# Kernel optimization log

Measured on AMD Instinct MI355X. Metric: run time of the kernel, lower is better.

## Reference

```python
import jax, jax.numpy as jnp
import numpy as np
from math import log

T, B, IN, H1, H2, OUT = 128, 256, 1024, 2048, 2048, 512
DT, INIT_TAU, MIN_TAU, THRESH, VREST = 0.01, 0.5, 0.1, 1.0, 0.0
SLOPE = 25.0  # snntorch surrogate.fast_sigmoid default slope

@jax.custom_vjp
def spike_fn(x):
    # Heaviside forward; fast-sigmoid surrogate backward
    return (x > 0).astype(x.dtype)

def _spike_fwd(x):
    return spike_fn(x), x

def _spike_bwd(x, g):
    return (g / (SLOPE * jnp.abs(x) + 1.0) ** 2,)

spike_fn.defvjp(_spike_fwd, _spike_bwd)

def setup_inputs() -> dict:
    key = jax.random.key(0)
    ks = jax.random.split(key, 7)
    init_w = -log(1.0 / (INIT_TAU - MIN_TAU) - 1.0)
    def lin(k, fan_in, fan_out):
        bound = 1.0 / np.sqrt(fan_in)
        kw, kb = jax.random.split(k)
        W = jax.random.uniform(kw, (fan_out, fan_in), jnp.float32, -bound, bound)
        b = jax.random.uniform(kb, (fan_out,), jnp.float32, -bound, bound)
        return W, b
    W1, b1 = lin(ks[0], IN, H1)
    W2, b2 = lin(ks[1], H1, H2)
    W3, b3 = lin(ks[2], H2, OUT)
    s = (jax.random.uniform(ks[3], (T, B, IN), jnp.float32) < 0.2).astype(jnp.float32)
    return {
        "s": s,
        "W1": W1, "b1": b1, "wt1": jnp.full((H1,), init_w, jnp.float32),
        "W2": W2, "b2": b2, "wt2": jnp.full((H2,), init_w, jnp.float32),
        "W3": W3, "b3": b3, "wt3": jnp.full((OUT,), init_w, jnp.float32),
    }

def _lif(v, cur, w_tau):
    tau = MIN_TAU + jax.nn.sigmoid(w_tau)
    v = v + (DT / tau) * (-(v - VREST) + cur)  # r = 1.0
    spike = spike_fn(v - THRESH)
    v_post = v * (1.0 - spike)  # zero reset
    return v_post, spike, v  # v is pre-reset membrane (v_tmp)

def reference(s, W1, b1, wt1, W2, b2, wt2, W3, b3, wt3):
    v0 = (jnp.zeros((B, H1), s.dtype), jnp.zeros((B, H2), s.dtype), jnp.zeros((B, OUT), s.dtype))
    def step(carry, st):
        v1, v2, v3 = carry
        v1, s1, _ = _lif(v1, st @ W1.T + b1, wt1)
        v2, s2, _ = _lif(v2, s1 @ W2.T + b2, wt2)
        v3, s3, vtmp = _lif(v3, s2 @ W3.T + b3, wt3)
        return (v1, v2, v3), (s3, vtmp)
    _, (out_s, out_v) = jax.lax.scan(step, v0, s)
    return out_s, out_v
```

## Files before the change

kernel.cpp:

```cpp
#include <hip/hip_runtime.h>
#include <hip/hip_bf16.h>
#include <cstdint>
#include <cstddef>

#define T_STEPS 128
#define BATCH   256
#define IN_F    1024
#define H1_F    2048
#define H2_F    2048
#define OUT_F   512
#define M_TOT   (T_STEPS * BATCH)

#define W1_SCALE 4064.0f
#define W1_INV   (1.0f / 4064.0f)

typedef __attribute__((ext_vector_type(4))) int   int4v;
typedef __attribute__((ext_vector_type(8))) unsigned short ushort8;
typedef unsigned long long ull;

__device__ __forceinline__ void load16_to_lds(const void* g, void* l) {
  __builtin_amdgcn_global_load_lds(
      (const __attribute__((address_space(1))) void*)g,
      (__attribute__((address_space(3))) void*)l, 16, 0, 0);
}

__device__ __forceinline__ unsigned short f2bf(float x) {
  __hip_bfloat16 h = __float2bfloat16(x);
  return *reinterpret_cast<unsigned short*>(&h);
}

__device__ __forceinline__ float bf2f(unsigned short u) {
  unsigned int w = ((unsigned int)u) << 16;
  return *reinterpret_cast<float*>(&w);
}

__device__ __forceinline__ float lif_k(float w) {
  float tau = 0.1f + 1.0f / (1.0f + expf(-w));
  return 0.01f / tau;
}

__global__ __launch_bounds__(256) void cvt_both(
    const float4* __restrict__ s_in, int4* __restrict__ s_out, int s16,
    const float4* __restrict__ w_in, int4* __restrict__ w_out, int w16) {
  int i = threadIdx.x + blockIdx.x * 256;
  bool is_s = (i < s16);
  const float4* in;
  int4* out;
  if (is_s) { in = s_in + (size_t)i * 4; out = s_out + i; }
  else {
    int j = i - s16;
    if (j >= w16) return;
    in = w_in + (size_t)j * 4; out = w_out + j;
  }
  int4 o;
  int* op = (int*)&o;
#pragma unroll
  for (int q = 0; q < 4; ++q) {
    float4 v = in[q];
    int c0, c1, c2, c3;
    if (is_s) {
      c0 = v.x > 0.5f; c1 = v.y > 0.5f; c2 = v.z > 0.5f; c3 = v.w > 0.5f;
    } else {
      c0 = __float2int_rn(v.x * W1_SCALE); c1 = __float2int_rn(v.y * W1_SCALE);
      c2 = __float2int_rn(v.z * W1_SCALE); c3 = __float2int_rn(v.w * W1_SCALE);
    }
    op[q] = (c0 & 0xff) | ((c1 & 0xff) << 8) | ((c2 & 0xff) << 16) | ((c3 & 0xff) << 24);
  }
  *out = o;
}

union SMem {
  struct { uint4 lA[1024]; uint4 lB[1024]; } st;
  unsigned short tile[128 * 136];
};

__global__ __launch_bounds__(256) void gemm_scan(
    const int8_t* __restrict__ A, const int8_t* __restrict__ B,
    const float* __restrict__ b1, const float* __restrict__ wt1,
    ull* __restrict__ mask1) {
  __shared__ SMem sm;
  const int K = IN_F;
  const int tid = threadIdx.x, lane = tid & 63, wv = tid >> 6;
  const int wm = (wv & 1) * 64, wn = (wv >> 1) * 64;

  const int id = blockIdx.x;
  const int xcd = id & 7, j = id >> 3;
  const int bblk = xcd * 32 + (j >> 4);
  const int n0   = (j & 15) * 128;

  const int mk = lane & 15, grp = lane >> 4;

  int4v acc[4][4] = {};

  for (int kt = 0; kt < K; kt += 128) {
#pragma unroll
    for (int i = 0; i < 4; ++i) {
      int cellbase = (wv * 4 + i) * 64;
      int cell = cellbase + lane;
      int r  = cell >> 3;
      int kb = (cell & 7) ^ (r & 7);
      load16_to_lds(A + (size_t)(r * BATCH + bblk) * K + kt + kb * 16, &sm.st.lA[cellbase]);
      load16_to_lds(B + (size_t)(n0 + r) * K + kt + kb * 16, &sm.st.lB[cellbase]);
    }
    __syncthreads();
#pragma unroll
    for (int ks = 0; ks < 2; ++ks) {
      int4v af[4], bfr[4];
      const int kb = ks * 4 + grp;
#pragma unroll
      for (int f = 0; f < 4; ++f) {
        int m = wm + f * 16 + mk;
        af[f]  = *(const int4v*)&sm.st.lA[m * 8 + (kb ^ (m & 7))];
        int n = wn + f * 16 + mk;
        bfr[f] = *(const int4v*)&sm.st.lB[n * 8 + (kb ^ (n & 7))];
      }
#pragma unroll
      for (int i = 0; i < 4; ++i)
#pragma unroll
        for (int jj = 0; jj < 4; ++jj)
          acc[i][jj] = __builtin_amdgcn_mfma_i32_16x16x64_i8(af[i], bfr[jj], acc[i][jj], 0, 0, 0);
    }
    __syncthreads();
  }

#pragma unroll
  for (int jj = 0; jj < 4; ++jj) {
    const int h = wn + jj * 16 + mk;
#pragma unroll
    for (int i = 0; i < 4; ++i) {
      const int t0 = wm + i * 16 + grp * 4;
      uint2 pk;
      pk.x = ((unsigned int)f2bf((float)acc[i][jj][1] * W1_INV) << 16)
           | f2bf((float)acc[i][jj][0] * W1_INV);
      pk.y = ((unsigned int)f2bf((float)acc[i][jj][3] * W1_INV) << 16)
           | f2bf((float)acc[i][jj][2] * W1_INV);
      *(uint2*)&sm.tile[h * 136 + t0] = pk;
    }
  }
  __syncthreads();

  if (tid < 128) {
    const int h  = tid;
    const int hg = n0 + h;
    const int wv2 = tid >> 6;
    const int ln  = tid & 63;
    const float bias = b1[hg];
    const float k    = lif_k(wt1[hg]);
    const size_t wbase = (size_t)(n0 >> 6) + wv2;
    float v = 0.0f;
    for (int t8 = 0; t8 < T_STEPS; t8 += 8) {
      ushort8 pk = *(const ushort8*)&sm.tile[h * 136 + t8];
#pragma unroll
      for (int u = 0; u < 8; ++u) {
        v = fmaf(k, (bf2f(pk[u]) + bias) - v, v);
        bool sp = v > 1.0f;
        ull bm = __ballot(sp);
        if (ln == 0)
          mask1[((size_t)(t8 + u) * BATCH + bblk) * (H1_F / 64) + wbase] = bm;
        if (sp) v = 0.0f;
      }
    }
  }
}

__global__ __launch_bounds__(1024) void layer23_kernel(
    const ull* __restrict__ mask1,
    const float* __restrict__ W2, const float* __restrict__ b2, const float* __restrict__ wt2,
    const float* __restrict__ W3, const float* __restrict__ b3, const float* __restrict__ wt3,
    float* __restrict__ out_s, float* __restrict__ out_v) {
  __shared__ ull m1all[T_STEPS * 32];
  __shared__ ull m2sh[2][32];
  const int tid = threadIdx.x, b = blockIdx.x;
  const int lane = tid & 63, wv = tid >> 6;

  const float bias2a = b2[tid], bias2b = b2[tid + 1024];
  const float k2a = lif_k(wt2[tid]), k2b = lif_k(wt2[tid + 1024]);
  const float* W2a = W2 + (size_t)tid * H1_F;
  const float* W2b = W2 + (size_t)(tid + 1024) * H1_F;
  float v2a = 0.0f, v2b = 0.0f;

  float bias3 = 0.0f, k3 = 0.0f, v3 = 0.0f;
  const float* W3r = W3;
  if (wv < 8) {
    bias3 = b3[tid];
    k3 = lif_k(wt3[tid]);
    W3r = W3 + (size_t)tid * H2_F;
  }

#pragma unroll
  for (int u = 0; u < 4; ++u) {
    int idx = tid + u * 1024;
    m1all[idx] = mask1[((size_t)(idx >> 5) * BATCH + b) * 32 + (idx & 31)];
  }
  __syncthreads();

  for (int t = 0; t < T_STEPS; ++t) {
    ull wrd = (lane < 32) ? m1all[t * 32 + lane] : 0ull;

    float cura = bias2a, curb = bias2b;
    if (__ballot(wrd != 0ull)) {
      for (int wi = 0; wi < 32; ++wi) {
        ull m = __shfl(wrd, wi, 64);
        while (m) {
          int bit = __ffsll(m) - 1;
          m &= m - 1;
          int idx = wi * 64 + bit;
          cura += W2a[idx];
          curb += W2b[idx];
        }
      }
    }
    v2a = fmaf(k2a, cura - v2a, v2a);
    v2b = fmaf(k2b, curb - v2b, v2b);
    bool spa = v2a > 1.0f, spb = v2b > 1.0f;
    ull sa = __ballot(spa);
    ull sb = __ballot(spb);
    if (lane == 0) { m2sh[t & 1][wv] = sa; m2sh[t & 1][16 + wv] = sb; }
    if (spa) v2a = 0.0f;
    if (spb) v2b = 0.0f;
    __syncthreads();

    if (wv < 8) {
      ull w3m = (lane < 32) ? m2sh[t & 1][lane] : 0ull;
      float cur3 = bias3;
      if (__ballot(w3m != 0ull)) {
        for (int wi = 0; wi < 32; ++wi) {
          ull m = __shfl(w3m, wi, 64);
          while (m) {
            int bit = __ffsll(m) - 1;
            m &= m - 1;
            cur3 += W3r[wi * 64 + bit];
          }
        }
      }
      float vp = fmaf(k3, cur3 - v3, v3);
      bool sp = vp > 1.0f;
      size_t idx = (size_t)(t * BATCH + b) * OUT_F + tid;
      out_s[idx] = sp ? 1.0f : 0.0f;
      out_v[idx] = vp;
      v3 = sp ? 0.0f : vp;
    }
  }
}

extern "C" void kernel_launch(void* const* d_in, const int* in_sizes, int n_in,
                              void* d_out, int out_size, void* d_ws, size_t ws_size,
                              hipStream_t stream) {
  const float* s   = (const float*)d_in[0];
  const float* W1  = (const float*)d_in[1];
  const float* b1  = (const float*)d_in[2];
  const float* wt1 = (const float*)d_in[3];
  const float* W2  = (const float*)d_in[4];
  const float* b2  = (const float*)d_in[5];
  const float* wt2 = (const float*)d_in[6];
  const float* W3  = (const float*)d_in[7];
  const float* b3  = (const float*)d_in[8];
  const float* wt3 = (const float*)d_in[9];

  char* wsb = (char*)d_ws;
  const size_t MASK_BYTES = (size_t)T_STEPS * BATCH * (H1_F / 64) * 8;
  const size_t S_ELEMS  = (size_t)M_TOT * IN_F;
  const size_t W1_ELEMS = (size_t)H1_F * IN_F;
  ull* mask1 = (ull*)wsb;
  int8_t* s_i8  = (int8_t*)(wsb + MASK_BYTES);
  int8_t* W1_i8 = s_i8 + S_ELEMS;
  (void)ws_size;

  float* outs = (float*)d_out;
  float* outv = outs + (size_t)T_STEPS * BATCH * OUT_F;

  const int s16 = (int)(S_ELEMS / 16), w16 = (int)(W1_ELEMS / 16);
  cvt_both<<<(s16 + w16 + 255) / 256, 256, 0, stream>>>(
      (const float4*)s, (int4*)s_i8, s16, (const float4*)W1, (int4*)W1_i8, w16);

  gemm_scan<<<BATCH * (H1_F / 128), 256, 0, stream>>>(s_i8, W1_i8, b1, wt1, mask1);

  layer23_kernel<<<BATCH, 1024, 0, stream>>>(mask1, W2, b2, wt2, W3, b3, wt3, outs, outv);
}
```

Before: 382.0 us.

## Double GEMM tile M to two batch columns per block, reusing W1 tile

Each gemm_scan block now covers two batch indices (256 time-rows) against the same 128 hidden units, so every W1 tile loaded into LDS is reused twice and the grid is halved. Each wave now holds 8x4 MFMA accumulators, and all 256 threads run the LIF scan afterwards instead of only 128. This roughly halves redundant B-operand traffic and makes better use of threads during the serial scan. In exchange it raises register and LDS pressure (launch_bounds 256,2), which may lower occupancy.

```diff
diff --git a/kernel.cpp b/kernel.cpp
--- a/kernel.cpp
+++ b/kernel.cpp
@@ -70,52 +70,63 @@
 }
 
 union SMem {
-  struct { uint4 lA[1024]; uint4 lB[1024]; } st;
-  unsigned short tile[128 * 136];
+  struct { uint4 lA[2048]; uint4 lB[1024]; } st;
+  unsigned short tile[2 * 128 * 136];
 };
 
-__global__ __launch_bounds__(256) void gemm_scan(
+__global__ __launch_bounds__(256, 2) void gemm_scan(
     const int8_t* __restrict__ A, const int8_t* __restrict__ B,
     const float* __restrict__ b1, const float* __restrict__ wt1,
     ull* __restrict__ mask1) {
   __shared__ SMem sm;
   const int K = IN_F;
   const int tid = threadIdx.x, lane = tid & 63, wv = tid >> 6;
-  const int wm = (wv & 1) * 64, wn = (wv >> 1) * 64;
+  const int wm = (wv & 1) * 128, wn = (wv >> 1) * 64;
 
   const int id = blockIdx.x;
   const int xcd = id & 7, j = id >> 3;
-  const int bblk = xcd * 32 + (j >> 4);
+  const int bblk = (xcd * 16 + (j >> 4)) * 2;
   const int n0   = (j & 15) * 128;
 
   const int mk = lane & 15, grp = lane >> 4;
 
-  int4v acc[4][4] = {};
+  int4v acc[8][4] = {};
 
   for (int kt = 0; kt < K; kt += 128) {
 #pragma unroll
-    for (int i = 0; i < 4; ++i) {
-      int cellbase = (wv * 4 + i) * 64;
+    for (int i = 0; i < 12; ++i) {
+      int cellbase = wv * 768 + i * 64;
       int cell = cellbase + lane;
-      int r  = cell >> 3;
-      int kb = (cell & 7) ^ (r & 7);
-      load16_to_lds(A + (size_t)(r * BATCH + bblk) * K + kt + kb * 16, &sm.st.lA[cellbase]);
-      load16_to_lds(B + (size_t)(n0 + r) * K + kt + kb * 16, &sm.st.lB[cellbase]);
+      if (cellbase < 2048) {
+        int r  = cell >> 3;
+        int kb = (cell & 7) ^ (r & 7);
+        load16_to_lds(A + (size_t)((r & 127) * BATCH + bblk + (r >> 7)) * K + kt + kb * 16,
+                      &sm.st.lA[cellbase]);
+      } else {
+        int c2 = cell - 2048;
+        int r  = c2 >> 3;
+        int kb = (c2 & 7) ^ (r & 7);
+        load16_to_lds(B + (size_t)(n0 + r) * K + kt + kb * 16,
+                      &sm.st.lB[cellbase - 2048]);
+      }
     }
     __syncthreads();
 #pragma unroll
     for (int ks = 0; ks < 2; ++ks) {
-      int4v af[4], bfr[4];
+      int4v af[8], bfr[4];
       const int kb = ks * 4 + grp;
 #pragma unroll
+      for (int f = 0; f < 8; ++f) {
+        int m = wm + f * 16 + mk;
+        af[f] = *(const int4v*)&sm.st.lA[m * 8 + (kb ^ (m & 7))];
+      }
+#pragma unroll
       for (int f = 0; f < 4; ++f) {
-        int m = wm + f * 16 + mk;
-        af[f]  = *(const int4v*)&sm.st.lA[m * 8 + (kb ^ (m & 7))];
         int n = wn + f * 16 + mk;
         bfr[f] = *(const int4v*)&sm.st.lB[n * 8 + (kb ^ (n & 7))];
       }
 #pragma unroll
-      for (int i = 0; i < 4; ++i)
+      for (int i = 0; i < 8; ++i)
 #pragma unroll
         for (int jj = 0; jj < 4; ++jj)
           acc[i][jj] = __builtin_amdgcn_mfma_i32_16x16x64_i8(af[i], bfr[jj], acc[i][jj], 0, 0, 0);
@@ -123,40 +134,46 @@
     __syncthreads();
   }
 
-#pragma unroll
-  for (int jj = 0; jj < 4; ++jj) {
-    const int h = wn + jj * 16 + mk;
-#pragma unroll
-    for (int i = 0; i < 4; ++i) {
-      const int t0 = wm + i * 16 + grp * 4;
-      uint2 pk;
-      pk.x = ((unsigned int)f2bf((float)acc[i][jj][1] * W1_INV) << 16)
-           | f2bf((float)acc[i][jj][0] * W1_INV);
-      pk.y = ((unsigned int)f2bf((float)acc[i][jj][3] * W1_INV) << 16)
-           | f2bf((float)acc[i][jj][2] * W1_INV);
-      *(uint2*)&sm.tile[h * 136 + t0] = pk;
+  {
+    const int b_sub = wv & 1;
+#pragma unroll
+    for (int jj = 0; jj < 4; ++jj) {
+      const int h = wn + jj * 16 + mk;
+      unsigned short* row = &sm.tile[(b_sub * 128 + h) * 136];
+#pragma unroll
+      for (int i = 0; i < 8; ++i) {
+        const int t0 = i * 16 + grp * 4;
+        uint2 pk;
+        pk.x = ((unsigned int)f2bf((float)acc[i][jj][1] * W1_INV) << 16)
+             | f2bf((float)acc[i][jj][0] * W1_INV);
+        pk.y = ((unsigned int)f2bf((float)acc[i][jj][3] * W1_INV) << 16)
+             | f2bf((float)acc[i][jj][2] * W1_INV);
+        *(uint2*)&row[t0] = pk;
+      }
     }
   }
   __syncthreads();
 
-  if (tid < 128) {
-    const int h  = tid;
+  {
+    const int b_sub = tid >> 7, h = tid & 127;
     const int hg = n0 + h;
-    const int wv2 = tid >> 6;
-    const int ln  = tid & 63;
+    const int ln = tid & 63;
+    const int word = (tid >> 6) & 1;
     const float bias = b1[hg];
     const float k    = lif_k(wt1[hg]);
-    const size_t wbase = (size_t)(n0 >> 6) + wv2;
+    const unsigned short* row = &sm.tile[(b_sub * 128 + h) * 136];
+    const size_t wbase = (size_t)(n0 >> 6) + word;
+    const int bg = bblk + b_sub;
     float v = 0.0f;
     for (int t8 = 0; t8 < T_STEPS; t8 += 8) {
-      ushort8 pk = *(const ushort8*)&sm.tile[h * 136 + t8];
+      ushort8 pk = *(const ushort8*)&row[t8];
 #pragma unroll
       for (int u = 0; u < 8; ++u) {
         v = fmaf(k, (bf2f(pk[u]) + bias) - v, v);
         bool sp = v > 1.0f;
         ull bm = __ballot(sp);
         if (ln == 0)
-          mask1[((size_t)(t8 + u) * BATCH + bblk) * (H1_F / 64) + wbase] = bm;
+          mask1[((size_t)(t8 + u) * BATCH + bg) * (H1_F / 64) + wbase] = bm;
         if (sp) v = 0.0f;
       }
     }
@@ -273,7 +290,7 @@
   cvt_both<<<(s16 + w16 + 255) / 256, 256, 0, stream>>>(
       (const float4*)s, (int4*)s_i8, s16, (const float4*)W1, (int4*)W1_i8, w16);
 
-  gemm_scan<<<BATCH * (H1_F / 128), 256, 0, stream>>>(s_i8, W1_i8, b1, wt1, mask1);
+  gemm_scan<<<(BATCH / 2) * (H1_F / 128), 256, 0, stream>>>(s_i8, W1_i8, b1, wt1, mask1);
 
   layer23_kernel<<<BATCH, 1024, 0, stream>>>(mask1, W2, b2, wt2, W3, b3, wt3, outs, outv);
 }
```

After: 378.1 us. About the same (-1.0%).
